# Kernel tuning notes

Measured on AMD Instinct MI355X. Metric: run time of the kernel, lower is better.

## Reference

```python
import jax, jax.numpy as jnp
import numpy as np

N = 20000    # num_nodes
E = 640000   # num_edges (avg degree 32)
D = 64       # hidden_dim (= input_dim = output_dim)


def setup_inputs() -> dict:
    key = jax.random.key(0)
    ks = jax.random.split(key, 8)
    x = jax.random.normal(ks[0], (N, D), dtype=jnp.float32)
    edge_index = jax.random.randint(ks[1], (2, E), 0, N, dtype=jnp.int32)
    # per-node hypernetwork-generated weights (scaled ~0.1 like weight_scales init)
    w0 = jax.random.normal(ks[2], (N, D, D), dtype=jnp.float32) * 0.05
    a0 = jax.random.normal(ks[3], (N, 2 * D, 1), dtype=jnp.float32) * 0.05
    b0 = jax.random.normal(ks[4], (N, D), dtype=jnp.float32) * 0.05
    w1 = jax.random.normal(ks[5], (N, D, D), dtype=jnp.float32) * 0.05
    a1 = jax.random.normal(ks[6], (N, 2 * D, 1), dtype=jnp.float32) * 0.05
    b1 = jax.random.normal(ks[7], (N, D), dtype=jnp.float32) * 0.05
    return {"x": x, "edge_index": edge_index,
            "w0": w0, "a0": a0, "b0": b0,
            "w1": w1, "a1": a1, "b1": b1}


def _gat_layer(x, edge_index, weight, att_weight, bias):
    # per-node linear: bmm(x.unsqueeze(1), weight).squeeze(1)
    h = jnp.einsum('ni,nio->no', x, weight)          # [N, D]
    row, col = edge_index[0], edge_index[1]
    h_i = h[row]                                     # [E, D] source
    h_j = h[col]                                     # [E, D] dest
    att_in = jnp.concatenate([h_i, h_j], axis=1)     # [E, 2D]
    a_src = att_weight[row, :, 0]                    # [E, 2D] per-source att vec
    scores = jnp.sum(att_in * a_src, axis=1)         # [E]
    scores = jax.nn.leaky_relu(scores, negative_slope=0.2)
    # segment softmax over destination nodes (replaces the unique(col) loop)
    seg_max = jax.ops.segment_max(scores, col, num_segments=N)  # [N]
    ex = jnp.exp(scores - seg_max[col])              # [E]
    seg_sum = jax.ops.segment_sum(ex, col, num_segments=N)      # [N]
    att = ex / seg_sum[col]                          # [E]
    msg = h_i * att[:, None]                         # [E, D]
    out = jax.ops.segment_sum(msg, col, num_segments=N)         # [N, D]
    return out + bias


def reference(x, edge_index, w0, a0, b0, w1, a1, b1):
    h = _gat_layer(x, edge_index, w0, a0, b0)
    h = jax.nn.relu(h)  # ReLU between layers; dropout is eval no-op
    out = _gat_layer(h, edge_index, w1, a1, b1)
    return out
```

## Files before the change

### kernel.cpp

```cpp
#include <hip/hip_runtime.h>
#include <math.h>

#define NN 20000
#define EE 640000
#define DD 64


__global__ __launch_bounds__(256) void k_zero(int* __restrict__ deg) {
  int i = blockIdx.x * 256 + threadIdx.x;
  if (i < NN) deg[i] = 0;
}

__global__ __launch_bounds__(256) void k_count(const int* __restrict__ col, int* __restrict__ deg) {
  int e = blockIdx.x * 256 + threadIdx.x;
  if (e < EE) atomicAdd(&deg[col[e]], 1);
}

__global__ __launch_bounds__(1024) void k_scan(const int* __restrict__ deg,
                                               int* __restrict__ offs,
                                               int* __restrict__ cursor) {
  __shared__ int part[1024];
  int t = threadIdx.x;
  const int CH = (NN + 1023) / 1024;
  int base = t * CH;
  int sum = 0;
  for (int i = 0; i < CH; ++i) {
    int idx = base + i;
    if (idx < NN) sum += deg[idx];
  }
  part[t] = sum;
  __syncthreads();
  for (int off = 1; off < 1024; off <<= 1) {
    int v = (t >= off) ? part[t - off] : 0;
    __syncthreads();
    part[t] += v;
    __syncthreads();
  }
  int run = (t == 0) ? 0 : part[t - 1];
  for (int i = 0; i < CH; ++i) {
    int idx = base + i;
    if (idx < NN) {
      offs[idx] = run;
      cursor[idx] = run;
      run += deg[idx];
    }
  }
  if (t == 1023) offs[NN] = part[1023];
}

__global__ __launch_bounds__(256) void k_scatter(const int* __restrict__ row,
                                                 const int* __restrict__ col,
                                                 int* __restrict__ cursor,
                                                 int* __restrict__ src) {
  int e = blockIdx.x * 256 + threadIdx.x;
  if (e < EE) {
    int pos = atomicAdd(&cursor[col[e]], 1);
    src[pos] = row[e];
  }
}


__global__ __launch_bounds__(256) void gat_h(const float* __restrict__ xin,
                                             const float* __restrict__ w,
                                             const float* __restrict__ a,
                                             float* __restrict__ h,
                                             float* __restrict__ s_self,
                                             int relu_in) {
  int n = (blockIdx.x * 256 + threadIdx.x) >> 6;
  int lane = threadIdx.x & 63;

  float xv = xin[(size_t)n * DD + lane];
  if (relu_in) xv = fmaxf(xv, 0.f);

  const float4* w4 = (const float4*)(w + (size_t)n * DD * DD);
  int oq = lane & 15;
  int isub = lane >> 4;
  float4 acc = make_float4(0.f, 0.f, 0.f, 0.f);
#pragma unroll
  for (int ib = 0; ib < 16; ++ib) {
    float4 wv = w4[ib * 64 + lane];
    float xi = __shfl(xv, ib * 4 + isub);
    acc.x += xi * wv.x;
    acc.y += xi * wv.y;
    acc.z += xi * wv.z;
    acc.w += xi * wv.w;
  }
#pragma unroll
  for (int m = 16; m <= 32; m <<= 1) {
    acc.x += __shfl_xor(acc.x, m);
    acc.y += __shfl_xor(acc.y, m);
    acc.z += __shfl_xor(acc.z, m);
    acc.w += __shfl_xor(acc.w, m);
  }
  if (lane < 16) {
    *(float4*)(h + (size_t)n * DD + oq * 4) = acc;
  }
  const float4* a4 = (const float4*)(a + (size_t)n * 2 * DD);
  float4 av = a4[oq];
  float p = acc.x * av.x + acc.y * av.y + acc.z * av.z + acc.w * av.w;
  if (lane >= 16) p = 0.f;
#pragma unroll
  for (int m = 1; m < 64; m <<= 1) p += __shfl_xor(p, m);
  if (lane == 0) s_self[n] = p;
}


__global__ __launch_bounds__(256) void gat_agg(const float* __restrict__ h,
                                               const float* __restrict__ s_self,
                                               const float* __restrict__ a,
                                               const int* __restrict__ offs,
                                               const int* __restrict__ src,
                                               const float* __restrict__ bias,
                                               float* __restrict__ out) {
  int widx = threadIdx.x >> 6;
  int lane = threadIdx.x & 63;
  int n = blockIdx.x * 4 + widx;
  int g = lane >> 4;
  int q = lane & 15;

  float4 hn = *(const float4*)(h + (size_t)n * DD + q * 4);

  int s0 = offs[n], s1 = offs[n + 1];
  float4 acc = make_float4(0.f, 0.f, 0.f, 0.f);
  float ssum = 0.f;

  int s = s0 + g;
  int r = (s < s1) ? src[s] : 0;
  for (int base = s0; base < s1; base += 4) {
    bool valid = (base + g) < s1;
    int rc = r;
    const float4* a2 = (const float4*)(a + (size_t)rc * 2 * DD + DD);
    float4 av = a2[q];
    float4 hr = *(const float4*)(h + (size_t)rc * DD + q * 4);
    float sself = s_self[rc];
    int snext = base + 4 + g;
    r = (snext < s1) ? src[snext] : 0;
    float p = av.x * hn.x + av.y * hn.y + av.z * hn.z + av.w * hn.w;
    p += __shfl_xor(p, 1);
    p += __shfl_xor(p, 2);
    p += __shfl_xor(p, 4);
    p += __shfl_xor(p, 8);
    float sc = sself + p;
    sc = sc > 0.f ? sc : 0.2f * sc;
    float ex = valid ? __expf(sc) : 0.f;
    acc.x += ex * hr.x;
    acc.y += ex * hr.y;
    acc.z += ex * hr.z;
    acc.w += ex * hr.w;
    ssum += ex;
  }
#pragma unroll
  for (int m = 16; m <= 32; m <<= 1) {
    acc.x += __shfl_xor(acc.x, m);
    acc.y += __shfl_xor(acc.y, m);
    acc.z += __shfl_xor(acc.z, m);
    acc.w += __shfl_xor(acc.w, m);
    ssum += __shfl_xor(ssum, m);
  }
  if (lane < 16) {
    float4 b4 = *(const float4*)(bias + (size_t)n * DD + q * 4);
    float inv = (s1 > s0) ? 1.f / ssum : 0.f;
    float4 o;
    o.x = b4.x + acc.x * inv;
    o.y = b4.y + acc.y * inv;
    o.z = b4.z + acc.z * inv;
    o.w = b4.w + acc.w * inv;
    *(float4*)(out + (size_t)n * DD + q * 4) = o;
  }
}


extern "C" void kernel_launch(void* const* d_in, const int* in_sizes, int n_in,
                              void* d_out, int out_size, void* d_ws, size_t ws_size,
                              hipStream_t stream) {
  const float* x = (const float*)d_in[0];
  const int* edge = (const int*)d_in[1];
  const float* w0 = (const float*)d_in[2];
  const float* a0 = (const float*)d_in[3];
  const float* b0 = (const float*)d_in[4];
  const float* w1 = (const float*)d_in[5];
  const float* a1 = (const float*)d_in[6];
  const float* b1 = (const float*)d_in[7];
  float* out = (float*)d_out;

  const int* row = edge;
  const int* col = edge + EE;

  char* p = (char*)d_ws;
  float* h = (float*)p;      p += (size_t)NN * DD * 4;
  float* s_self = (float*)p; p += (size_t)NN * 4;
  int* deg = (int*)p;        p += (size_t)NN * 4;
  int* offs = (int*)p;       p += (size_t)(NN + 1) * 4;
  int* cursor = (int*)p;     p += (size_t)NN * 4;
  int* src = (int*)p;        p += (size_t)EE * 4;

  k_zero<<<(NN + 255) / 256, 256, 0, stream>>>(deg);
  k_count<<<(EE + 255) / 256, 256, 0, stream>>>(col, deg);
  k_scan<<<1, 1024, 0, stream>>>(deg, offs, cursor);
  k_scatter<<<(EE + 255) / 256, 256, 0, stream>>>(row, col, cursor, src);

  gat_h<<<NN / 4, 256, 0, stream>>>(x, w0, a0, h, s_self, 0);
  gat_agg<<<NN / 4, 256, 0, stream>>>(h, s_self, a0, offs, src, b0, out);
  gat_h<<<NN / 4, 256, 0, stream>>>(out, w1, a1, h, s_self, 1);
  gat_agg<<<NN / 4, 256, 0, stream>>>(h, s_self, a1, offs, src, b1, out);
}
```

Before: 818.7 us.

## Overlap layer-0 per-node transform with CSR build kernels

The layer-0 per-node matrix-vector work is split across the count, scan and scatter kernels as extra blocks, so the small latency-bound CSR build steps share the GPU with the bandwidth-heavy weight streaming. Node ranges are 0-9000 in the count kernel, 9000-17000 in the scan kernel and 17000-20000 in the scatter kernel. Weight loads switch to nontemporal loads, and the zero kernel is replaced by a memset. The cost is hard-coded block partitions tied to N and E, and a scan kernel whose blocks now all run with 1024 threads.

```diff
diff --git a/kernel.cpp b/kernel.cpp
--- a/kernel.cpp
+++ b/kernel.cpp
@@ -5,80 +5,37 @@
 #define EE 640000
 #define DD 64
 
-
-__global__ __launch_bounds__(256) void k_zero(int* __restrict__ deg) {
-  int i = blockIdx.x * 256 + threadIdx.x;
-  if (i < NN) deg[i] = 0;
-}
-
-__global__ __launch_bounds__(256) void k_count(const int* __restrict__ col, int* __restrict__ deg) {
-  int e = blockIdx.x * 256 + threadIdx.x;
-  if (e < EE) atomicAdd(&deg[col[e]], 1);
-}
-
-__global__ __launch_bounds__(1024) void k_scan(const int* __restrict__ deg,
-                                               int* __restrict__ offs,
-                                               int* __restrict__ cursor) {
-  __shared__ int part[1024];
-  int t = threadIdx.x;
-  const int CH = (NN + 1023) / 1024;
-  int base = t * CH;
-  int sum = 0;
-  for (int i = 0; i < CH; ++i) {
-    int idx = base + i;
-    if (idx < NN) sum += deg[idx];
-  }
-  part[t] = sum;
-  __syncthreads();
-  for (int off = 1; off < 1024; off <<= 1) {
-    int v = (t >= off) ? part[t - off] : 0;
-    __syncthreads();
-    part[t] += v;
-    __syncthreads();
-  }
-  int run = (t == 0) ? 0 : part[t - 1];
-  for (int i = 0; i < CH; ++i) {
-    int idx = base + i;
-    if (idx < NN) {
-      offs[idx] = run;
-      cursor[idx] = run;
-      run += deg[idx];
-    }
-  }
-  if (t == 1023) offs[NN] = part[1023];
-}
-
-__global__ __launch_bounds__(256) void k_scatter(const int* __restrict__ row,
-                                                 const int* __restrict__ col,
-                                                 int* __restrict__ cursor,
-                                                 int* __restrict__ src) {
-  int e = blockIdx.x * 256 + threadIdx.x;
-  if (e < EE) {
-    int pos = atomicAdd(&cursor[col[e]], 1);
-    src[pos] = row[e];
-  }
-}
-
-
-__global__ __launch_bounds__(256) void gat_h(const float* __restrict__ xin,
-                                             const float* __restrict__ w,
-                                             const float* __restrict__ a,
-                                             float* __restrict__ h,
-                                             float* __restrict__ s_self,
-                                             int relu_in) {
-  int n = (blockIdx.x * 256 + threadIdx.x) >> 6;
-  int lane = threadIdx.x & 63;
-
+#define CNT_BLK 2500
+#define K1_HBLK 2250
+#define K2_NODE0 9000
+#define K2_HBLK 500
+#define K3_NODE0 17000
+#define K3_HBLK 750
+
+typedef float f4v __attribute__((ext_vector_type(4)));
+__device__ __forceinline__ float4 nt_load4(const float* p) {
+  f4v v = __builtin_nontemporal_load((const f4v*)p);
+  return make_float4(v.x, v.y, v.z, v.w);
+}
+
+
+__device__ __forceinline__ void gat_h_node(int n, int lane,
+                                           const float* __restrict__ xin,
+                                           const float* __restrict__ w,
+                                           const float* __restrict__ a,
+                                           float* __restrict__ h,
+                                           float* __restrict__ s_self,
+                                           int relu_in) {
   float xv = xin[(size_t)n * DD + lane];
   if (relu_in) xv = fmaxf(xv, 0.f);
 
-  const float4* w4 = (const float4*)(w + (size_t)n * DD * DD);
+  const float* wbase = w + (size_t)n * DD * DD;
   int oq = lane & 15;
   int isub = lane >> 4;
   float4 acc = make_float4(0.f, 0.f, 0.f, 0.f);
 #pragma unroll
   for (int ib = 0; ib < 16; ++ib) {
-    float4 wv = w4[ib * 64 + lane];
+    float4 wv = nt_load4(wbase + (size_t)(ib * 64 + lane) * 4);
     float xi = __shfl(xv, ib * 4 + isub);
     acc.x += xi * wv.x;
     acc.y += xi * wv.y;
@@ -102,6 +59,97 @@
 #pragma unroll
   for (int m = 1; m < 64; m <<= 1) p += __shfl_xor(p, m);
   if (lane == 0) s_self[n] = p;
+}
+
+
+__global__ __launch_bounds__(256) void k1_count_h(const int* __restrict__ col,
+                                                  int* __restrict__ deg,
+                                                  const float* __restrict__ x,
+                                                  const float* __restrict__ w0,
+                                                  const float* __restrict__ a0,
+                                                  float* __restrict__ h,
+                                                  float* __restrict__ s_self) {
+  if (blockIdx.x < CNT_BLK) {
+    int e = blockIdx.x * 256 + threadIdx.x;
+    atomicAdd(&deg[col[e]], 1);
+  } else {
+    int n = ((int)blockIdx.x - CNT_BLK) * 4 + (threadIdx.x >> 6);
+    gat_h_node(n, threadIdx.x & 63, x, w0, a0, h, s_self, 0);
+  }
+}
+
+
+__global__ __launch_bounds__(1024) void k2_scan_h(const int* __restrict__ deg,
+                                                  int* __restrict__ offs,
+                                                  int* __restrict__ cursor,
+                                                  const float* __restrict__ x,
+                                                  const float* __restrict__ w0,
+                                                  const float* __restrict__ a0,
+                                                  float* __restrict__ h,
+                                                  float* __restrict__ s_self) {
+  if (blockIdx.x == 0) {
+    __shared__ int part[1024];
+    int t = threadIdx.x;
+    const int CH = (NN + 1023) / 1024;
+    int base = t * CH;
+    int sum = 0;
+    for (int i = 0; i < CH; ++i) {
+      int idx = base + i;
+      if (idx < NN) sum += deg[idx];
+    }
+    part[t] = sum;
+    __syncthreads();
+    for (int off = 1; off < 1024; off <<= 1) {
+      int v = (t >= off) ? part[t - off] : 0;
+      __syncthreads();
+      part[t] += v;
+      __syncthreads();
+    }
+    int run = (t == 0) ? 0 : part[t - 1];
+    for (int i = 0; i < CH; ++i) {
+      int idx = base + i;
+      if (idx < NN) {
+        offs[idx] = run;
+        cursor[idx] = run;
+        run += deg[idx];
+      }
+    }
+    if (t == 1023) offs[NN] = part[1023];
+  } else {
+    int n = K2_NODE0 + ((int)blockIdx.x - 1) * 16 + ((int)threadIdx.x >> 6);
+    gat_h_node(n, threadIdx.x & 63, x, w0, a0, h, s_self, 0);
+  }
+}
+
+
+__global__ __launch_bounds__(256) void k3_scatter_h(const int* __restrict__ row,
+                                                    const int* __restrict__ col,
+                                                    int* __restrict__ cursor,
+                                                    int* __restrict__ src,
+                                                    const float* __restrict__ x,
+                                                    const float* __restrict__ w0,
+                                                    const float* __restrict__ a0,
+                                                    float* __restrict__ h,
+                                                    float* __restrict__ s_self) {
+  if (blockIdx.x < CNT_BLK) {
+    int e = blockIdx.x * 256 + threadIdx.x;
+    int pos = atomicAdd(&cursor[col[e]], 1);
+    src[pos] = row[e];
+  } else {
+    int n = K3_NODE0 + ((int)blockIdx.x - CNT_BLK) * 4 + (threadIdx.x >> 6);
+    gat_h_node(n, threadIdx.x & 63, x, w0, a0, h, s_self, 0);
+  }
+}
+
+
+__global__ __launch_bounds__(256) void gat_h_k(const float* __restrict__ xin,
+                                               const float* __restrict__ w,
+                                               const float* __restrict__ a,
+                                               float* __restrict__ h,
+                                               float* __restrict__ s_self,
+                                               int relu_in) {
+  int n = ((int)blockIdx.x * 256 + (int)threadIdx.x) >> 6;
+  gat_h_node(n, threadIdx.x & 63, xin, w, a, h, s_self, relu_in);
 }
 
 
@@ -194,13 +242,13 @@
   int* cursor = (int*)p;     p += (size_t)NN * 4;
   int* src = (int*)p;        p += (size_t)EE * 4;
 
-  k_zero<<<(NN + 255) / 256, 256, 0, stream>>>(deg);
-  k_count<<<(EE + 255) / 256, 256, 0, stream>>>(col, deg);
-  k_scan<<<1, 1024, 0, stream>>>(deg, offs, cursor);
-  k_scatter<<<(EE + 255) / 256, 256, 0, stream>>>(row, col, cursor, src);
-
-  gat_h<<<NN / 4, 256, 0, stream>>>(x, w0, a0, h, s_self, 0);
+  hipMemsetAsync(deg, 0, (size_t)NN * 4, stream);
+
+  k1_count_h<<<CNT_BLK + K1_HBLK, 256, 0, stream>>>(col, deg, x, w0, a0, h, s_self);
+  k2_scan_h<<<1 + K2_HBLK, 1024, 0, stream>>>(deg, offs, cursor, x, w0, a0, h, s_self);
+  k3_scatter_h<<<CNT_BLK + K3_HBLK, 256, 0, stream>>>(row, col, cursor, src, x, w0, a0, h, s_self);
+
   gat_agg<<<NN / 4, 256, 0, stream>>>(h, s_self, a0, offs, src, b0, out);
-  gat_h<<<NN / 4, 256, 0, stream>>>(out, w1, a1, h, s_self, 1);
+  gat_h_k<<<NN / 4, 256, 0, stream>>>(out, w1, a1, h, s_self, 1);
   gat_agg<<<NN / 4, 256, 0, stream>>>(h, s_self, a1, offs, src, b1, out);
 }
```

After: 790.1 us. -3.5%, faster.
